# Optimization experiments

Hardware: AMD Instinct MI355X
Metric: run time of the kernel (lower is better)

Reference implementation:

```python
import jax, jax.numpy as jnp
import numpy as np

B, N, C = 256, 196, 384
H, KD, VD = 8, 32, 128  # num_heads, key_dim, val_dim (attn_ratio*key_dim)
RES = 14
SCALE = KD ** -0.5


def _make_bias_idxs():
    # Reproduce the LeViT relative-position index buffer deterministically.
    ii, jj = np.meshgrid(np.arange(RES), np.arange(RES), indexing='ij')
    pos = np.stack([ii.reshape(-1), jj.reshape(-1)])  # [2, N]
    rel = np.abs(pos[:, :, None] - pos[:, None, :])   # [2, N, N]
    return jnp.asarray(rel[0] * RES + rel[1], dtype=jnp.int32)  # [N, N]


def setup_inputs() -> dict:
    key = jax.random.key(0)
    ks = jax.random.split(key, 6)
    s_in = 1.0 / np.sqrt(C)
    s_v = 1.0 / np.sqrt(H * VD)
    return {
        'x': jax.random.normal(ks[0], (B, N, C), jnp.float32),
        'w_qkv': jax.random.normal(ks[1], (2 * H * KD + H * VD, C), jnp.float32) * s_in,
        'b_qkv': jax.random.normal(ks[2], (2 * H * KD + H * VD,), jnp.float32) * 0.01,
        'w_proj': jax.random.normal(ks[3], (C, H * VD), jnp.float32) * s_v,
        'b_proj': jax.random.normal(ks[4], (C,), jnp.float32) * 0.01,
        'attn_biases': jax.random.normal(ks[5], (H, RES * RES), jnp.float32) * 0.02,
        'bias_idxs': _make_bias_idxs(),
    }


def reference(x, w_qkv, b_qkv, w_proj, b_proj, attn_biases, bias_idxs):
    Bb, Nn, _ = x.shape
    qkv = x @ w_qkv.T + b_qkv                       # [B, N, 2*H*KD + H*VD]
    qkv = qkv.reshape(Bb, Nn, H, 2 * KD + VD).transpose(0, 2, 1, 3)  # [B, H, N, .]
    q, k, v = qkv[..., :KD], qkv[..., KD:2 * KD], qkv[..., 2 * KD:]
    bias = attn_biases[:, bias_idxs]                # [H, N, N] gathered per head
    attn = jnp.einsum('bhnd,bhmd->bhnm', q, k) * SCALE + bias
    attn = jax.nn.softmax(attn, axis=-1)
    out = jnp.einsum('bhnm,bhmd->bhnd', attn, v)    # [B, H, N, VD]
    out = out.transpose(0, 2, 1, 3).reshape(Bb, Nn, H * VD)
    return out @ w_proj.T + b_proj                  # [B, N, C]
```

## Files before the change

### kernel.cpp

```cpp
#include <hip/hip_runtime.h>

typedef unsigned short u16;
typedef short short8 __attribute__((ext_vector_type(8)));
typedef float f32x4 __attribute__((ext_vector_type(4)));
typedef __bf16 bf16x8 __attribute__((ext_vector_type(8)));

#define SCALE_QK 0.17677669529663687f

__device__ __forceinline__ u16 f2b(float f) {
    unsigned int u = __builtin_bit_cast(unsigned int, f);
    u += 0x7fffu + ((u >> 16) & 1u);
    return (u16)(u >> 16);
}

__device__ __forceinline__ f32x4 mfma16(short8 a, short8 b, f32x4 c) {
    return __builtin_amdgcn_mfma_f32_16x16x32_bf16(
        __builtin_bit_cast(bf16x8, a), __builtin_bit_cast(bf16x8, b), c, 0, 0, 0);
}

__device__ __forceinline__ void gload_lds16(const u16* g, u16* l) {
    __builtin_amdgcn_global_load_lds(
        (const __attribute__((address_space(1))) unsigned int*)g,
        (__attribute__((address_space(3))) unsigned int*)l, 16, 0, 0);
}

__device__ __forceinline__ int xcd_swizzle(int bid, int nwg) {
    int qd = nwg >> 3, rm = nwg & 7;
    int xcd = bid & 7, lo = bid >> 3;
    return (xcd < rm ? xcd * (qd + 1) : rm * (qd + 1) + (xcd - rm) * qd) + lo;
}

__global__ void cvt_kernel(const float4* __restrict__ in, ushort4* __restrict__ out, int n4) {
    int stride = gridDim.x * blockDim.x;
    for (int i = blockIdx.x * blockDim.x + threadIdx.x; i < n4; i += stride) {
        float4 v = in[i];
        ushort4 o;
        o.x = f2b(v.x); o.y = f2b(v.y); o.z = f2b(v.z); o.w = f2b(v.w);
        out[i] = o;
    }
}

__global__ void biasmat_kernel(const float* __restrict__ ab, const int* __restrict__ idxs,
                               float* __restrict__ bm) {
    int total = 8 * 196 * 196;
    int stride = gridDim.x * blockDim.x;
    for (int i = blockIdx.x * blockDim.x + threadIdx.x; i < total; i += stride) {
        int h = i / (196 * 196);
        int ij = i - h * (196 * 196);
        bm[i] = ab[h * 196 + idxs[ij]];
    }
}

template <int KDIM, int NTILES, int EPI>
__global__ __launch_bounds__(256) void gemm_kernel(
    const u16* __restrict__ A, const u16* __restrict__ Bw, const float* __restrict__ bias,
    u16* __restrict__ o_q, u16* __restrict__ o_k, u16* __restrict__ o_v,
    float* __restrict__ o_f) {
    __shared__ u16 Asl[3][128 * 32];
    __shared__ u16 Bsl[3][128 * 32];

    const int wg = xcd_swizzle(blockIdx.x, gridDim.x);
    const int tm = wg / NTILES, tn = wg % NTILES;
    const int tid = threadIdx.x, wave = tid >> 6, lane = tid & 63;
    const int l15 = lane & 15, l4 = lane >> 4;
    const int wm = (wave >> 1) * 64, wn = (wave & 1) * 64;

    const u16* Ab = A + (size_t)tm * 128 * KDIM;
    const u16* Bb = Bw + (size_t)tn * 128 * KDIM;

    f32x4 acc[4][4] = {};

    auto stage = [&](int buf, int k0) {
#pragma unroll
        for (int i = 0; i < 2; i++) {
            int row = wave * 32 + i * 16 + (lane >> 2);
            int sc = (lane & 3) ^ ((row >> 1) & 3);
            gload_lds16(Ab + (size_t)row * KDIM + k0 + sc * 8,
                        &Asl[buf][(wave * 32 + i * 16) * 32]);
            gload_lds16(Bb + (size_t)row * KDIM + k0 + sc * 8,
                        &Bsl[buf][(wave * 32 + i * 16) * 32]);
        }
    };

    constexpr int NT = KDIM / 32;
    stage(0, 0);
    stage(1, 32);
#pragma unroll
    for (int t = 0; t < NT; ++t) {
        if (t + 2 < NT) {
            stage((t + 2) % 3, (t + 2) * 32);
            asm volatile("s_waitcnt vmcnt(8)" ::: "memory");
        } else if (t + 1 < NT) {
            asm volatile("s_waitcnt vmcnt(4)" ::: "memory");
        } else {
            asm volatile("s_waitcnt vmcnt(0)" ::: "memory");
        }
        __builtin_amdgcn_s_barrier();

        const char* As = (const char*)Asl[t % 3];
        const char* Bs = (const char*)Bsl[t % 3];
        short8 af[4], bfr[4];
#pragma unroll
        for (int u = 0; u < 4; u++) {
            int rowa = wm + u * 16 + l15;
            int bytea = rowa * 64 + ((l4 * 16) ^ (((rowa >> 1) & 3) << 4));
            af[u] = *reinterpret_cast<const short8*>(As + bytea);
            int rowb = wn + u * 16 + l15;
            int byteb = rowb * 64 + ((l4 * 16) ^ (((rowb >> 1) & 3) << 4));
            bfr[u] = *reinterpret_cast<const short8*>(Bs + byteb);
        }
        __builtin_amdgcn_s_setprio(1);
#pragma unroll
        for (int mt = 0; mt < 4; mt++)
#pragma unroll
            for (int nt = 0; nt < 4; nt++)
                acc[mt][nt] = mfma16(af[mt], bfr[nt], acc[mt][nt]);
        __builtin_amdgcn_s_setprio(0);
        __builtin_amdgcn_s_barrier();
    }

#pragma unroll
    for (int mt = 0; mt < 4; mt++) {
#pragma unroll
        for (int nt = 0; nt < 4; nt++) {
            int gn = tn * 128 + wn + nt * 16 + l15;
            float bv = bias[gn];
#pragma unroll
            for (int r = 0; r < 4; r++) {
                int gm = tm * 128 + wm + mt * 16 + l4 * 4 + r;
                float v = acc[mt][nt][r] + bv;
                if (EPI == 0) {
                    int bb = gm / 196, nn = gm - bb * 196;
                    int h = gn / 192, r2 = gn - h * 192;
                    int bh = bb * 8 + h;
                    if (r2 < 32)
                        o_q[((size_t)bh * 196 + nn) * 32 + r2] = f2b(v);
                    else if (r2 < 64)
                        o_k[((size_t)bh * 196 + nn) * 32 + (r2 - 32)] = f2b(v);
                    else
                        o_v[((size_t)bh * 196 + nn) * 128 + (r2 - 64)] = f2b(v);
                } else {
                    o_f[(size_t)gm * 384 + gn] = v;
                }
            }
        }
    }
}

__global__ __launch_bounds__(512) void attn_kernel(
    const u16* __restrict__ qb, const u16* __restrict__ kb, const u16* __restrict__ vb,
    const float* __restrict__ bm, u16* __restrict__ out) {
    __shared__ u16 Klds[224 * 40];
    __shared__ u16 Vlds[128 * 232];
    __shared__ u16 Plds[8][16 * 232];

    const int bh = blockIdx.x;
    const int b = bh >> 3, h = bh & 7;
    const int tid = threadIdx.x, wave = tid >> 6, lane = tid & 63;
    const int l15 = lane & 15, l4 = lane >> 4;

    for (int u = tid; u < 128 * 28; u += 512) {
        int rw = u / 28, c = u - rw * 28;
        Vlds[rw * 232 + 196 + c] = 0;
    }
    const u16* kbase = kb + (size_t)bh * (196 * 32);
    for (int u = tid; u < 896; u += 512) {
        int j = u >> 2, c8 = (u & 3) * 8;
        short8 v = {};
        if (j < 196) v = *reinterpret_cast<const short8*>(kbase + j * 32 + c8);
        *reinterpret_cast<short8*>(&Klds[j * 40 + c8]) = v;
    }
    const u16* vbase = vb + (size_t)bh * (196 * 128);
    for (int u0 = tid; u0 < 3136; u0 += 512) {
        int k = u0 >> 4;
        int d0 = (u0 & 15) * 8;
        short8 vv = *reinterpret_cast<const short8*>(vbase + k * 128 + d0);
#pragma unroll
        for (int jj = 0; jj < 8; jj++) {
            int j = (jj + lane) & 7;
            Vlds[(d0 + j) * 232 + k] = (u16)vv[j];
        }
    }
    __syncthreads();

    const float* bmh = bm + h * (196 * 196);
    const u16* qbase = qb + (size_t)bh * (196 * 32);
    u16* P = &Plds[wave][0];

    for (int it = wave; it < 13; it += 8) {
        int i0 = it * 16;
        int qn = i0 + l15; if (qn > 195) qn = 195;
        short8 qf = *reinterpret_cast<const short8*>(qbase + qn * 32 + l4 * 8);

        f32x4 s[13];
        __builtin_amdgcn_s_setprio(1);
#pragma unroll
        for (int jt = 0; jt < 13; jt++) {
            short8 kf = *reinterpret_cast<const short8*>(&Klds[(jt * 16 + l15) * 40 + l4 * 8]);
            f32x4 z = {0.f, 0.f, 0.f, 0.f};
            s[jt] = mfma16(qf, kf, z);
        }
        __builtin_amdgcn_s_setprio(0);

#pragma unroll
        for (int r = 0; r < 4; r++) {
            int gi = i0 + l4 * 4 + r;
            int girow = gi < 196 ? gi : 195;
            float mx = -3e38f;
#pragma unroll
            for (int jt = 0; jt < 13; jt++) {
                int gj = jt * 16 + l15;
                float v = (gj < 196) ? (s[jt][r] * SCALE_QK + bmh[girow * 196 + gj]) : -3e38f;
                s[jt][r] = v;
                mx = fmaxf(mx, v);
            }
            mx = fmaxf(mx, __shfl_xor(mx, 1));
            mx = fmaxf(mx, __shfl_xor(mx, 2));
            mx = fmaxf(mx, __shfl_xor(mx, 4));
            mx = fmaxf(mx, __shfl_xor(mx, 8));
            float sum = 0.f;
#pragma unroll
            for (int jt = 0; jt < 13; jt++) {
                float p = __expf(s[jt][r] - mx);
                s[jt][r] = p;
                sum += p;
            }
            sum += __shfl_xor(sum, 1);
            sum += __shfl_xor(sum, 2);
            sum += __shfl_xor(sum, 4);
            sum += __shfl_xor(sum, 8);
            float inv = 1.f / sum;
#pragma unroll
            for (int jt = 0; jt < 13; jt++) s[jt][r] *= inv;
        }

#pragma unroll
        for (int jt = 0; jt < 13; jt++) {
#pragma unroll
            for (int r = 0; r < 4; r++)
                P[(l4 * 4 + r) * 232 + jt * 16 + l15] = f2b(s[jt][r]);
        }
#pragma unroll
        for (int r = 0; r < 4; r++) P[(l4 * 4 + r) * 232 + 208 + l15] = 0;

        f32x4 o[8] = {};
#pragma unroll
        for (int ks = 0; ks < 7; ks++) {
            short8 pf = *reinterpret_cast<const short8*>(&P[l15 * 232 + ks * 32 + l4 * 8]);
            __builtin_amdgcn_s_setprio(1);
#pragma unroll
            for (int dt = 0; dt < 8; dt++) {
                short8 vf = *reinterpret_cast<const short8*>(
                    &Vlds[(dt * 16 + l15) * 232 + ks * 32 + l4 * 8]);
                o[dt] = mfma16(pf, vf, o[dt]);
            }
            __builtin_amdgcn_s_setprio(0);
        }

        u16* ob = out + ((size_t)b * 196) * 1024 + h * 128;
#pragma unroll
        for (int dt = 0; dt < 8; dt++) {
#pragma unroll
            for (int r = 0; r < 4; r++) {
                int gi = i0 + l4 * 4 + r;
                if (gi < 196) ob[(size_t)gi * 1024 + dt * 16 + l15] = f2b(o[dt][r]);
            }
        }
    }
}

extern "C" void kernel_launch(void* const* d_in, const int* in_sizes, int n_in,
                              void* d_out, int out_size, void* d_ws, size_t ws_size,
                              hipStream_t stream) {
    const float* x = (const float*)d_in[0];
    const float* w_qkv = (const float*)d_in[1];
    const float* b_qkv = (const float*)d_in[2];
    const float* w_proj = (const float*)d_in[3];
    const float* b_proj = (const float*)d_in[4];
    const float* attn_biases = (const float*)d_in[5];
    const int* bias_idxs = (const int*)d_in[6];
    float* out = (float*)d_out;

    const size_t MB = 1ull << 20;
    int nc;
    bool full_aout;
    if (ws_size >= 310 * MB)      { nc = 1; full_aout = true; }
    else if (ws_size >= 165 * MB) { nc = 4; full_aout = true; }
    else                          { nc = 4; full_aout = false; }
    const int cb = 256 / nc;
    const size_t chm = (size_t)cb * 196;
    const int chbh = cb * 8;

    char* p = (char*)d_ws;
    auto alloc = [&](size_t bytes) {
        void* r = (void*)p;
        p += (bytes + 255) & ~(size_t)255;
        return r;
    };
    u16* wqb = (u16*)alloc(1536ull * 384 * 2);
    u16* wpb = (u16*)alloc(384ull * 1024 * 2);
    float* bmat = (float*)alloc(8ull * 196 * 196 * 4);
    u16* xbc = (u16*)alloc(chm * 384 * 2);
    u16* qc = (u16*)alloc((size_t)chbh * 196 * 32 * 2);
    u16* kc = (u16*)alloc((size_t)chbh * 196 * 32 * 2);
    u16* vc = (u16*)alloc((size_t)chbh * 196 * 128 * 2);
    u16* aout_b = (u16*)alloc((full_aout ? 50176ull : chm) * 1024 * 2);

    cvt_kernel<<<576, 256, 0, stream>>>((const float4*)w_qkv, (ushort4*)wqb, 1536 * 384 / 4);
    cvt_kernel<<<384, 256, 0, stream>>>((const float4*)w_proj, (ushort4*)wpb, 384 * 1024 / 4);
    biasmat_kernel<<<1201, 256, 0, stream>>>(attn_biases, bias_idxs, bmat);

    const int qkv_grid = (int)(chm / 128) * 12;
    const int proj_grid_chunk = (int)(chm / 128) * 3;

    for (int c = 0; c < nc; ++c) {
        const float* xc = x + (size_t)c * chm * 384;
        cvt_kernel<<<1024, 256, 0, stream>>>((const float4*)xc, (ushort4*)xbc,
                                             (int)(chm * 384 / 4));
        gemm_kernel<384, 12, 0><<<qkv_grid, 256, 0, stream>>>(xbc, wqb, b_qkv, qc, kc, vc,
                                                              nullptr);
        u16* aoutc = aout_b + (full_aout ? (size_t)c * chm * 1024 : 0);
        attn_kernel<<<chbh, 512, 0, stream>>>(qc, kc, vc, bmat, aoutc);
        if (!full_aout) {
            gemm_kernel<1024, 3, 1><<<proj_grid_chunk, 256, 0, stream>>>(
                aoutc, wpb, b_proj, nullptr, nullptr, nullptr, out + (size_t)c * chm * 384);
        }
    }
    if (full_aout) {
        gemm_kernel<1024, 3, 1><<<392 * 3, 256, 0, stream>>>(aout_b, wpb, b_proj, nullptr,
                                                             nullptr, nullptr, out);
    }
}
```

Baseline: 380.9 us.

## Transpose QK^T MFMA and redistribute softmax probabilities via shuffles instead of LDS

Swaps the MFMA operands so each lane holds a query column of scores, which lets the softmax reductions use two cross-row shuffles instead of four per row. The probabilities are packed into bf16 pairs and redistributed to the PV MFMA A-operand layout with lane shuffles, removing the per-wave P staging buffer in LDS. The attention bias is now read with a stride of 196 floats per element, which gives less coalesced global loads. The launch-bounds hint now requests higher occupancy, made possible by the smaller LDS footprint.

```diff
diff --git a/kernel.cpp b/kernel.cpp
--- a/kernel.cpp
+++ b/kernel.cpp
@@ -1,9 +1,11 @@
 #include <hip/hip_runtime.h>
 
 typedef unsigned short u16;
+typedef unsigned int u32;
 typedef short short8 __attribute__((ext_vector_type(8)));
 typedef float f32x4 __attribute__((ext_vector_type(4)));
 typedef __bf16 bf16x8 __attribute__((ext_vector_type(8)));
+typedef unsigned int u32x4 __attribute__((ext_vector_type(4)));
 
 #define SCALE_QK 0.17677669529663687f
 
@@ -11,6 +13,10 @@
     unsigned int u = __builtin_bit_cast(unsigned int, f);
     u += 0x7fffu + ((u >> 16) & 1u);
     return (u16)(u >> 16);
+}
+
+__device__ __forceinline__ u32 pack2(float lo, float hi) {
+    return ((u32)f2b(hi) << 16) | (u32)f2b(lo);
 }
 
 __device__ __forceinline__ f32x4 mfma16(short8 a, short8 b, f32x4 c) {
@@ -147,12 +153,11 @@
     }
 }
 
-__global__ __launch_bounds__(512) void attn_kernel(
+__global__ __launch_bounds__(512, 4) void attn_kernel(
     const u16* __restrict__ qb, const u16* __restrict__ kb, const u16* __restrict__ vb,
     const float* __restrict__ bm, u16* __restrict__ out) {
     __shared__ u16 Klds[224 * 40];
     __shared__ u16 Vlds[128 * 232];
-    __shared__ u16 Plds[8][16 * 232];
 
     const int bh = blockIdx.x;
     const int b = bh >> 3, h = bh & 7;
@@ -185,12 +190,12 @@
 
     const float* bmh = bm + h * (196 * 196);
     const u16* qbase = qb + (size_t)bh * (196 * 32);
-    u16* P = &Plds[wave][0];
 
     for (int it = wave; it < 13; it += 8) {
         int i0 = it * 16;
-        int qn = i0 + l15; if (qn > 195) qn = 195;
-        short8 qf = *reinterpret_cast<const short8*>(qbase + qn * 32 + l4 * 8);
+        int q = i0 + l15;
+        int qcl = q < 196 ? q : 195;
+        short8 qf = *reinterpret_cast<const short8*>(qbase + qcl * 32 + l4 * 8);
 
         f32x4 s[13];
         __builtin_amdgcn_s_setprio(1);
@@ -198,61 +203,67 @@
         for (int jt = 0; jt < 13; jt++) {
             short8 kf = *reinterpret_cast<const short8*>(&Klds[(jt * 16 + l15) * 40 + l4 * 8]);
             f32x4 z = {0.f, 0.f, 0.f, 0.f};
-            s[jt] = mfma16(qf, kf, z);
+            s[jt] = mfma16(kf, qf, z);
         }
         __builtin_amdgcn_s_setprio(0);
 
-#pragma unroll
-        for (int r = 0; r < 4; r++) {
-            int gi = i0 + l4 * 4 + r;
-            int girow = gi < 196 ? gi : 195;
-            float mx = -3e38f;
-#pragma unroll
-            for (int jt = 0; jt < 13; jt++) {
-                int gj = jt * 16 + l15;
-                float v = (gj < 196) ? (s[jt][r] * SCALE_QK + bmh[girow * 196 + gj]) : -3e38f;
+        float mx = -3e38f;
+#pragma unroll
+        for (int jt = 0; jt < 13; jt++) {
+#pragma unroll
+            for (int r = 0; r < 4; r++) {
+                int gk = jt * 16 + l4 * 4 + r;
+                float v = (gk < 196) ? (s[jt][r] * SCALE_QK + bmh[gk * 196 + qcl]) : -3e38f;
                 s[jt][r] = v;
                 mx = fmaxf(mx, v);
             }
-            mx = fmaxf(mx, __shfl_xor(mx, 1));
-            mx = fmaxf(mx, __shfl_xor(mx, 2));
-            mx = fmaxf(mx, __shfl_xor(mx, 4));
-            mx = fmaxf(mx, __shfl_xor(mx, 8));
-            float sum = 0.f;
-#pragma unroll
-            for (int jt = 0; jt < 13; jt++) {
+        }
+        mx = fmaxf(mx, __shfl_xor(mx, 16));
+        mx = fmaxf(mx, __shfl_xor(mx, 32));
+        float sum = 0.f;
+#pragma unroll
+        for (int jt = 0; jt < 13; jt++) {
+#pragma unroll
+            for (int r = 0; r < 4; r++) {
                 float p = __expf(s[jt][r] - mx);
                 s[jt][r] = p;
                 sum += p;
             }
-            sum += __shfl_xor(sum, 1);
-            sum += __shfl_xor(sum, 2);
-            sum += __shfl_xor(sum, 4);
-            sum += __shfl_xor(sum, 8);
-            float inv = 1.f / sum;
-#pragma unroll
-            for (int jt = 0; jt < 13; jt++) s[jt][r] *= inv;
-        }
-
+        }
+        sum += __shfl_xor(sum, 16);
+        sum += __shfl_xor(sum, 32);
+        float inv = 1.f / sum;
+
+        u32 pk01[14], pk23[14];
 #pragma unroll
         for (int jt = 0; jt < 13; jt++) {
-#pragma unroll
-            for (int r = 0; r < 4; r++)
-                P[(l4 * 4 + r) * 232 + jt * 16 + l15] = f2b(s[jt][r]);
-        }
-#pragma unroll
-        for (int r = 0; r < 4; r++) P[(l4 * 4 + r) * 232 + 208 + l15] = 0;
+            pk01[jt] = pack2(s[jt][0] * inv, s[jt][1] * inv);
+            pk23[jt] = pack2(s[jt][2] * inv, s[jt][3] * inv);
+        }
+        pk01[13] = 0; pk23[13] = 0;
 
         f32x4 o[8] = {};
+        const int sl0 = l15 + ((l4 & 1) * 2) * 16;
+        const int sl1 = sl0 + 16;
+        const bool hi_jt = (l4 & 2) != 0;
 #pragma unroll
         for (int ks = 0; ks < 7; ks++) {
-            short8 pf = *reinterpret_cast<const short8*>(&P[l15 * 232 + ks * 32 + l4 * 8]);
+            u32 a0 = __shfl(pk01[ks * 2], sl0), a1 = __shfl(pk01[ks * 2 + 1], sl0);
+            u32 b0 = __shfl(pk23[ks * 2], sl0), b1 = __shfl(pk23[ks * 2 + 1], sl0);
+            u32 c0 = __shfl(pk01[ks * 2], sl1), c1 = __shfl(pk01[ks * 2 + 1], sl1);
+            u32 d0_ = __shfl(pk23[ks * 2], sl1), d1 = __shfl(pk23[ks * 2 + 1], sl1);
+            u32x4 pw;
+            pw.x = hi_jt ? a1 : a0;
+            pw.y = hi_jt ? b1 : b0;
+            pw.z = hi_jt ? c1 : c0;
+            pw.w = hi_jt ? d1 : d0_;
+            short8 pa = __builtin_bit_cast(short8, pw);
             __builtin_amdgcn_s_setprio(1);
 #pragma unroll
             for (int dt = 0; dt < 8; dt++) {
                 short8 vf = *reinterpret_cast<const short8*>(
                     &Vlds[(dt * 16 + l15) * 232 + ks * 32 + l4 * 8]);
-                o[dt] = mfma16(pf, vf, o[dt]);
+                o[dt] = mfma16(pa, vf, o[dt]);
             }
             __builtin_amdgcn_s_setprio(0);
         }
```

Measured after the change: 1.012 ms. 2.66x slower.
